# Optimization experiments

Hardware: AMD Instinct MI355X
Metric: run time of the kernel (lower is better)

## Reference

```python
import jax, jax.numpy as jnp
import numpy as np

TEMPERATURE = 0.1

def setup_inputs() -> dict:
    key = jax.random.key(0)
    k1, k2 = jax.random.split(key)
    z_i = jax.random.normal(k1, (4096, 128), dtype=jnp.float32)
    z_j = jax.random.normal(k2, (4096, 128), dtype=jnp.float32)
    return {"z_i": z_i, "z_j": z_j}

def reference(z_i, z_j):
    n = z_i.shape[0]
    reps = jnp.concatenate([z_i, z_j], axis=0)              # (2N, D)
    # cosine similarity via normalize + GEMM (same math as broadcasted CosineSimilarity,
    # torch eps=1e-8 on the norm)
    norms = jnp.maximum(jnp.linalg.norm(reps, axis=1, keepdims=True), 1e-8)
    rn = reps / norms
    sim = rn @ rn.T                                          # (2N, 2N)
    l_pos = jnp.diagonal(sim, offset=n)                      # (N,)
    r_pos = jnp.diagonal(sim, offset=-n)                     # (N,)
    positives = jnp.concatenate([l_pos, r_pos])[:, None]     # (2N, 1)
    # NOTE: original code's mask bug makes `negatives` the FULL sim matrix
    logits = jnp.concatenate([positives, sim], axis=1) / TEMPERATURE  # (2N, 2N+1)
    # cross-entropy with label 0, reduction='sum'
    log_probs = jax.nn.log_softmax(logits, axis=1)
    loss = -jnp.sum(log_probs[:, 0])
    return loss / (2 * n)
```

## Files before the change

kernel.cpp:

```cpp
#include <hip/hip_runtime.h>
#include <hip/hip_bf16.h>

typedef __bf16 bf16x8 __attribute__((ext_vector_type(8)));
typedef __bf16 bf16x2 __attribute__((ext_vector_type(2)));
typedef float f32x4 __attribute__((ext_vector_type(4)));

#define NROWS 8192
#define HALF_N 4096
#define DIM 128
#define C1 14.42695040888963f
#define LN2 0.6931471805599453f
#define GBLK 1024


__global__ __launch_bounds__(256) void k_normalize(
    const float* __restrict__ zi, const float* __restrict__ zj,
    char* __restrict__ packA, char* __restrict__ packB,
    float* __restrict__ rowsum, float* __restrict__ pbuf,
    unsigned int* __restrict__ done)
{
    const int wave = threadIdx.x >> 6;
    const int lane = threadIdx.x & 63;
    const int ks_  = lane >> 4;
    const int qr_  = (lane >> 2) & 3;
    const int rem_ = (lane & 3) * 4;
    #pragma unroll
    for (int t = 0; t < 2; ++t) {
        const int idx = blockIdx.x * 8 + wave * 2 + t;
        float2 vi = *(const float2*)(zi + (size_t)idx * DIM + lane * 2);
        float2 vj = *(const float2*)(zj + (size_t)idx * DIM + lane * 2);
        float ssi = vi.x * vi.x + vi.y * vi.y;
        float ssj = vj.x * vj.x + vj.y * vj.y;
        float cr  = vi.x * vj.x + vi.y * vj.y;
        #pragma unroll
        for (int m = 32; m >= 1; m >>= 1) {
            ssi += __shfl_xor(ssi, m, 64);
            ssj += __shfl_xor(ssj, m, 64);
            cr  += __shfl_xor(cr,  m, 64);
        }
        const float sci = 1.0f / fmaxf(sqrtf(ssi), 1e-8f);
        const float scj = 1.0f / fmaxf(sqrtf(ssj), 1e-8f);
        #pragma unroll
        for (int h = 0; h < 2; ++h) {
            const int   row = idx + h * HALF_N;
            const float sx  = h ? vj.x * scj : vi.x * sci;
            const float sy  = h ? vj.y * scj : vi.y * sci;
            const size_t off = (size_t)(row >> 4) * 4096 + ks_ * 1024
                             + (qr_ * 16 + (row & 15)) * 16 + rem_;
            bf16x2 a, b;
            a[0] = (__bf16)(sx * C1); a[1] = (__bf16)(sy * C1);
            b[0] = (__bf16)sx;        b[1] = (__bf16)sy;
            *(bf16x2*)(packA + off) = a;
            *(bf16x2*)(packB + off) = b;
        }
        if (lane == 0) {
            const float p = cr * sci * scj;
            pbuf[idx] = p;
            pbuf[idx + HALF_N] = p;
        }
    }
    if (threadIdx.x < 16) rowsum[blockIdx.x * 16 + threadIdx.x] = 0.0f;
    if (blockIdx.x == 0 && threadIdx.x == 0) *done = 0u;
}

__global__ __launch_bounds__(256, 4) void k_gemm(
    const char* __restrict__ packA, const char* __restrict__ packB,
    float* __restrict__ rowsum, const float* __restrict__ pbuf,
    unsigned int* __restrict__ done, float* __restrict__ out)
{
    const int wave = threadIdx.x >> 6;
    const int lane = threadIdx.x & 63;
    const int qrow = lane >> 4, lcol = lane & 15;
    const int cv = blockIdx.x & 31;
    const int rg = (blockIdx.x >> 5) * 4 + wave;

    bf16x8 afrag[4][4];
    #pragma unroll
    for (int mi = 0; mi < 4; ++mi)
        #pragma unroll
        for (int ks = 0; ks < 4; ++ks)
            afrag[mi][ks] = *(const bf16x8*)(packA
                + (size_t)(rg * 4 + mi) * 4096 + ks * 1024 + lane * 16);

    float rsum[4][4];
    #pragma unroll
    for (int mi = 0; mi < 4; ++mi)
        #pragma unroll
        for (int r = 0; r < 4; ++r) rsum[mi][r] = 0.0f;

    const char* Bb = packB + (size_t)(cv * 16) * 4096 + lane * 16;

    #pragma unroll 1
    for (int s = 0; s < 16; ++s) {
        const char* bp = Bb + (size_t)s * 4096;
        bf16x8 bfrag[4];
        #pragma unroll
        for (int ks = 0; ks < 4; ++ks)
            bfrag[ks] = *(const bf16x8*)(bp + ks * 1024);

        f32x4 acc[4];
        const f32x4 zero = {0.0f, 0.0f, 0.0f, 0.0f};
        #pragma unroll
        for (int mi = 0; mi < 4; ++mi) acc[mi] = zero;
        #pragma unroll
        for (int ks = 0; ks < 4; ++ks)
            #pragma unroll
            for (int mi = 0; mi < 4; ++mi)
                acc[mi] = __builtin_amdgcn_mfma_f32_16x16x32_bf16(
                    afrag[mi][ks], bfrag[ks], acc[mi], 0, 0, 0);

        #pragma unroll
        for (int mi = 0; mi < 4; ++mi)
            #pragma unroll
            for (int r = 0; r < 4; ++r)
                rsum[mi][r] += __builtin_amdgcn_exp2f(acc[mi][r]);
    }

    #pragma unroll
    for (int mi = 0; mi < 4; ++mi)
        #pragma unroll
        for (int r = 0; r < 4; ++r) {
            float v = rsum[mi][r];
            v += __shfl_xor(v, 1, 64);
            v += __shfl_xor(v, 2, 64);
            v += __shfl_xor(v, 4, 64);
            v += __shfl_xor(v, 8, 64);
            if (lcol == 0)
                atomicAdd(&rowsum[rg * 64 + mi * 16 + qrow * 4 + r], v);
        }

    __syncthreads();
    __shared__ int is_last;
    if (threadIdx.x == 0) {
        unsigned old = __hip_atomic_fetch_add(done, 1u, __ATOMIC_RELAXED,
                                              __HIP_MEMORY_SCOPE_AGENT);
        is_last = (old == GBLK - 1);
    }
    __syncthreads();
    if (!is_last) return;
    __threadfence();

    float lsum = 0.0f;
    for (int r = threadIdx.x; r < NROWS; r += 256) {
        float rs = __hip_atomic_load(&rowsum[r], __ATOMIC_RELAXED, __HIP_MEMORY_SCOPE_AGENT);
        float pc = pbuf[r] * C1;
        float S  = rs + __builtin_amdgcn_exp2f(pc);
        lsum += (__builtin_amdgcn_logf(S) - pc) * LN2;
    }
    #pragma unroll
    for (int m = 32; m >= 1; m >>= 1) lsum += __shfl_xor(lsum, m, 64);
    __shared__ float part[4];
    if (lane == 0) part[wave] = lsum;
    __syncthreads();
    if (threadIdx.x == 0)
        out[0] = (part[0] + part[1] + part[2] + part[3]) * (1.0f / (float)NROWS);
}

extern "C" void kernel_launch(void* const* d_in, const int* in_sizes, int n_in,
                              void* d_out, int out_size, void* d_ws, size_t ws_size,
                              hipStream_t stream)
{
    const float* zi = (const float*)d_in[0];
    const float* zj = (const float*)d_in[1];
    float* out = (float*)d_out;

    char*  packA  = (char*)d_ws;
    char*  packB  = packA + (size_t)NROWS * 256;
    float* rowsum = (float*)(packB + (size_t)NROWS * 256);
    float* pbuf   = rowsum + NROWS;
    unsigned int* done = (unsigned int*)(pbuf + NROWS);

    k_normalize<<<NROWS / 16, 256, 0, stream>>>(zi, zj, packA, packB, rowsum, pbuf, done);
    k_gemm<<<GBLK, 256, 0, stream>>>(packA, packB, rowsum, pbuf, done, out);
}
```

Baseline: 99.60 us.

## Shrink per-wave row tile to 16 rows and launch 4x more GEMM blocks

Each wave now handles one 16-row A tile instead of four, so the grid grows from 1024 to 4096 blocks and launch bounds allow 8 blocks per CU. This cuts register pressure and raises occupancy and parallelism to hide load and exp latency. In exchange, every B fragment is reused by only one MFMA instead of four, so B traffic from memory or cache grows fourfold, and atomics and the final-block counter are spread over more blocks.

```diff
diff --git a/kernel.cpp b/kernel.cpp
--- a/kernel.cpp
+++ b/kernel.cpp
@@ -10,7 +10,7 @@
 #define DIM 128
 #define C1 14.42695040888963f
 #define LN2 0.6931471805599453f
-#define GBLK 1024
+#define GBLK 4096
 
 
 __global__ __launch_bounds__(256) void k_normalize(
@@ -63,7 +63,7 @@
     if (blockIdx.x == 0 && threadIdx.x == 0) *done = 0u;
 }
 
-__global__ __launch_bounds__(256, 4) void k_gemm(
+__global__ __launch_bounds__(256, 8) void k_gemm(
     const char* __restrict__ packA, const char* __restrict__ packB,
     float* __restrict__ rowsum, const float* __restrict__ pbuf,
     unsigned int* __restrict__ done, float* __restrict__ out)
@@ -74,20 +74,13 @@
     const int cv = blockIdx.x & 31;
     const int rg = (blockIdx.x >> 5) * 4 + wave;
 
-    bf16x8 afrag[4][4];
+    const char* Ab = packA + (size_t)rg * 4096 + lane * 16;
+    bf16x8 afrag[4];
     #pragma unroll
-    for (int mi = 0; mi < 4; ++mi)
-        #pragma unroll
-        for (int ks = 0; ks < 4; ++ks)
-            afrag[mi][ks] = *(const bf16x8*)(packA
-                + (size_t)(rg * 4 + mi) * 4096 + ks * 1024 + lane * 16);
+    for (int ks = 0; ks < 4; ++ks)
+        afrag[ks] = *(const bf16x8*)(Ab + ks * 1024);
 
-    float rsum[4][4];
-    #pragma unroll
-    for (int mi = 0; mi < 4; ++mi)
-        #pragma unroll
-        for (int r = 0; r < 4; ++r) rsum[mi][r] = 0.0f;
-
+    float rsum[4] = {0.0f, 0.0f, 0.0f, 0.0f};
     const char* Bb = packB + (size_t)(cv * 16) * 4096 + lane * 16;
 
     #pragma unroll 1
@@ -98,36 +91,27 @@
         for (int ks = 0; ks < 4; ++ks)
             bfrag[ks] = *(const bf16x8*)(bp + ks * 1024);
 
-        f32x4 acc[4];
-        const f32x4 zero = {0.0f, 0.0f, 0.0f, 0.0f};
-        #pragma unroll
-        for (int mi = 0; mi < 4; ++mi) acc[mi] = zero;
+        f32x4 acc = {0.0f, 0.0f, 0.0f, 0.0f};
         #pragma unroll
         for (int ks = 0; ks < 4; ++ks)
-            #pragma unroll
-            for (int mi = 0; mi < 4; ++mi)
-                acc[mi] = __builtin_amdgcn_mfma_f32_16x16x32_bf16(
-                    afrag[mi][ks], bfrag[ks], acc[mi], 0, 0, 0);
+            acc = __builtin_amdgcn_mfma_f32_16x16x32_bf16(
+                afrag[ks], bfrag[ks], acc, 0, 0, 0);
 
         #pragma unroll
-        for (int mi = 0; mi < 4; ++mi)
-            #pragma unroll
-            for (int r = 0; r < 4; ++r)
-                rsum[mi][r] += __builtin_amdgcn_exp2f(acc[mi][r]);
+        for (int r = 0; r < 4; ++r)
+            rsum[r] += __builtin_amdgcn_exp2f(acc[r]);
     }
 
     #pragma unroll
-    for (int mi = 0; mi < 4; ++mi)
-        #pragma unroll
-        for (int r = 0; r < 4; ++r) {
-            float v = rsum[mi][r];
-            v += __shfl_xor(v, 1, 64);
-            v += __shfl_xor(v, 2, 64);
-            v += __shfl_xor(v, 4, 64);
-            v += __shfl_xor(v, 8, 64);
-            if (lcol == 0)
-                atomicAdd(&rowsum[rg * 64 + mi * 16 + qrow * 4 + r], v);
-        }
+    for (int r = 0; r < 4; ++r) {
+        float v = rsum[r];
+        v += __shfl_xor(v, 1, 64);
+        v += __shfl_xor(v, 2, 64);
+        v += __shfl_xor(v, 4, 64);
+        v += __shfl_xor(v, 8, 64);
+        if (lcol == 0)
+            atomicAdd(&rowsum[rg * 16 + qrow * 4 + r], v);
+    }
 
     __syncthreads();
     __shared__ int is_last;
```

Measured after the change: 142.7 us. +43.2%, slower.
